# Kernel tuning notes

Hardware: AMD Instinct MI355X
Metric: run time of the kernel (lower is better)

Reference implementation:

```python
import jax, jax.numpy as jnp
import numpy as np
from jax import lax

G, K, C_IN, C_FEAT, H, W, B = 8, 6, 512, 256, 64, 64, 1


def apply_offset(offset):
    # offset: [N, 2, H, W] pixel-space offsets -> sampling grid [N, H, W, 2] in [-1, 1]
    # channel 0 displaces x (width), channel 1 displaces y (height), matching the
    # reversed-meshgrid logic of the original torch apply_offset.
    n, _, h, w = offset.shape
    jj = jnp.arange(w, dtype=offset.dtype)[None, None, :]
    ii = jnp.arange(h, dtype=offset.dtype)[None, :, None]
    gx = (jj + offset[:, 0]) / ((w - 1.0) / 2.0) - 1.0
    gy = (ii + offset[:, 1]) / ((h - 1.0) / 2.0) - 1.0
    return jnp.stack([gx, gy], axis=-1)


def grid_sample_border(img, grid):
    # img: [N, C, H, W], grid: [N, H, W, 2] in [-1, 1]
    # Bilinear, padding_mode='border', align_corners=False (torch grid_sample default).
    n, c, h, w = img.shape
    x = jnp.clip((grid[..., 0] + 1.0) * w * 0.5 - 0.5, 0.0, w - 1.0)
    y = jnp.clip((grid[..., 1] + 1.0) * h * 0.5 - 0.5, 0.0, h - 1.0)
    x0 = jnp.floor(x)
    y0 = jnp.floor(y)
    wx = (x - x0)[:, None]  # [N,1,H,W]
    wy = (y - y0)[:, None]
    x0i = x0.astype(jnp.int32)
    y0i = y0.astype(jnp.int32)
    x1i = jnp.minimum(x0i + 1, w - 1)
    y1i = jnp.minimum(y0i + 1, h - 1)

    def gather(im, yi, xi):  # im [C,H,W]; yi, xi [H,W]
        return im[:, yi, xi]

    g = jax.vmap(gather)
    v00 = g(img, y0i, x0i)
    v01 = g(img, y0i, x1i)
    v10 = g(img, y1i, x0i)
    v11 = g(img, y1i, x1i)
    return (1.0 - wy) * ((1.0 - wx) * v00 + wx * v01) + wy * ((1.0 - wx) * v10 + wx * v11)


def setup_inputs() -> dict:
    key = jax.random.key(0)
    ks = jax.random.split(key, 11)
    s = 0.02
    return {
        "gar_feat": jax.random.normal(ks[0], (B, C_FEAT, H, W), jnp.float32),
        "cond_feat": jax.random.normal(ks[1], (B, C_FEAT, H, W), jnp.float32),
        "mask": jax.random.uniform(ks[2], (B, G, C_FEAT), dtype=jnp.float32),
        "W1": jax.random.normal(ks[3], (G, 128, C_IN, 3, 3), jnp.float32) * s,
        "b1": jax.random.normal(ks[4], (G, 128), jnp.float32) * s,
        "W2": jax.random.normal(ks[5], (G, 64, 128, 3, 3), jnp.float32) * s,
        "b2": jax.random.normal(ks[6], (G, 64), jnp.float32) * s,
        "W3": jax.random.normal(ks[7], (G, 32, 64, 3, 3), jnp.float32) * s,
        "b3": jax.random.normal(ks[8], (G, 32), jnp.float32) * s,
        "W4": jax.random.normal(ks[9], (G, 3 * K, 32, 3, 3), jnp.float32) * s,
        "b4": jax.random.normal(ks[10], (G, 3 * K), jnp.float32) * s,
    }


def reference(gar_feat, cond_feat, mask, W1, b1, W2, b2, W3, b3, W4, b4):
    b, c, h, w = gar_feat.shape
    g = W1.shape[0]
    k = W4.shape[1] // 3
    inp = jnp.concatenate([gar_feat, cond_feat], axis=1)  # [B, 2C, H, W]

    def conv(x, wgt, bias):
        return lax.conv_general_dilated(
            x, wgt, (1, 1), 'SAME', dimension_numbers=('NCHW', 'OIHW', 'NCHW')
        ) + bias[None, :, None, None]

    def lrelu(x):
        return jnp.where(x >= 0, x, 0.1 * x)

    def group_net(w1, bb1, w2, bb2, w3, bb3, w4, bb4):
        hid = lrelu(conv(inp, w1, bb1))
        hid = lrelu(conv(hid, w2, bb2))
        hid = lrelu(conv(hid, w3, bb3))
        return conv(hid, w4, bb4)  # [B, 3k, H, W]

    oa = jax.vmap(group_net)(W1, b1, W2, b2, W3, b3, W4, b4)  # [G, B, 3k, H, W]
    attn = jax.nn.softmax(oa[:, :, 2 * k:], axis=0)           # softmax across groups: [G,B,k,H,W]
    off = oa[:, :, :2 * k].reshape(g, b * k, 2, h, w)
    grid = jax.vmap(apply_offset)(off)                        # [G, B*k, H, W, 2]

    rep = jnp.repeat(gar_feat, k, axis=0)                     # [B*k, C, H, W]

    def warp_group(grid_g, attn_g, mask_g):
        samp = grid_sample_border(rep, grid_g).reshape(b, k, c, h, w)
        wfeat = jnp.sum(samp * attn_g[:, :, None], axis=1)    # [B, C, H, W]
        return wfeat * mask_g[:, :, None, None]

    warped = jax.vmap(warp_group)(grid, attn, jnp.transpose(mask, (1, 0, 2)))
    return jnp.sum(warped, axis=0)  # [B, C, H, W]
```

## Files before the change

kernel.cpp:

```cpp
#include <hip/hip_runtime.h>
#include <hip/hip_bf16.h>

typedef __hip_bfloat16 bf16;
typedef unsigned short ushort8v __attribute__((ext_vector_type(8)));
typedef short  s16x4  __attribute__((ext_vector_type(4)));
typedef short  bf16x8 __attribute__((ext_vector_type(8)));
typedef float  f32x4  __attribute__((ext_vector_type(4)));

#define HW 4096
#define IMG_W 64

__device__ __forceinline__ float bfbits2f(unsigned short u) {
    return __uint_as_float(((unsigned int)u) << 16);
}
__device__ __forceinline__ short f2bs(float f) {
    bf16 h = __float2bfloat16(f);
    return *reinterpret_cast<short*>(&h);
}

__device__ __forceinline__ void gl_lds16(const void* g, void* s) {
    __builtin_amdgcn_global_load_lds(
        (const __attribute__((address_space(1))) unsigned int*)g,
        (__attribute__((address_space(3))) unsigned int*)s, 16, 0, 0);
}

__device__ void pack_input_dev(const float* __restrict__ gar,
                               const float* __restrict__ cond,
                               short* __restrict__ outp, int bx2, float* tile)
{
    int bx = bx2 & 127;
    int by = bx2 >> 7;
    int tx = threadIdx.x & 31;
    int ty = threadIdx.x >> 5;
#pragma unroll
    for (int i = 0; i < 4; ++i) {
        int c = by * 32 + ty + i * 8;
        const float* src = (c < 256) ? (gar + (size_t)c * HW)
                                     : (cond + (size_t)(c - 256) * HW);
        tile[(ty + i * 8) * 33 + tx] = src[bx * 32 + tx];
    }
    __syncthreads();
#pragma unroll
    for (int i = 0; i < 4; ++i) {
        int p = bx * 32 + ty + i * 8;
        outp[((size_t)by * 4096 + p) * 32 + tx] = f2bs(tile[tx * 33 + ty + i * 8]);
    }
}

template<int CIN, int CREAL, int BN, int NT, bool COAL>
__device__ void pack_w_dev(const float* __restrict__ wgt, char* __restrict__ wp,
                           int bx, short* sT)
{
    constexpr int NCC  = CIN / 32;
    constexpr int BLKB = 9 * 4 * BN * 16;

    const int t  = threadIdx.x;
    const int cc = bx % NCC;
    const int nt = (bx / NCC) % NT;
    const int g  = bx / (NT * NCC);

    for (int i = t; i < BLKB / 8; i += 256)
        reinterpret_cast<s16x4*>(sT)[i] = s16x4{0, 0, 0, 0};
    __syncthreads();

    int ocmax = CREAL - nt * BN; if (ocmax > BN) ocmax = BN;
    const size_t base = ((size_t)(g * CREAL + nt * BN) * CIN + cc * 32) * 9;
    for (int i = t; i < ocmax * 288; i += 256) {
        int oc = i / 288;
        int r  = i % 288;
        int ic = r / 9, tap = r % 9;
        size_t idx;
        if (COAL) idx = (size_t)(((tap * BN + oc) * 4 + (ic >> 3)) * 8 + (ic & 7));
        else      idx = (size_t)(((tap * 4 + (ic >> 3)) * BN + oc) * 8 + (ic & 7));
        sT[idx] = f2bs(wgt[base + (size_t)oc * CIN * 9 + r]);
    }
    __syncthreads();

    const s16x4* src = reinterpret_cast<const s16x4*>(sT);
    s16x4* dst = reinterpret_cast<s16x4*>(wp + (size_t)bx * BLKB);
    for (int i = t; i < BLKB / 8; i += 256)
        dst[i] = src[i];
}

__global__ __launch_bounds__(256)
void pack_all(const float* __restrict__ gar, const float* __restrict__ cond,
              const float* __restrict__ W1, const float* __restrict__ W2,
              const float* __restrict__ W3, const float* __restrict__ W4,
              short* inp_t, char* W1p, char* W2p, char* W3p, char* W4p)
{
    __shared__ __align__(16) short sbuf[9 * 4 * 64 * 8];
    int bx = blockIdx.x;
    if (bx < 256)      pack_w_dev<512, 128, 64, 2, true >(W1, W1p, bx,       sbuf);
    else if (bx < 288) pack_w_dev<128,  64, 64, 1, false>(W2, W2p, bx - 256, sbuf);
    else if (bx < 304) pack_w_dev< 64,  32, 32, 1, false>(W3, W3p, bx - 288, sbuf);
    else if (bx < 312) pack_w_dev< 32,  18, 32, 1, false>(W4, W4p, bx - 304, sbuf);
    else pack_input_dev(gar, cond, inp_t, bx - 312, (float*)sbuf);
}

template<int ICP, int CREAL, int BN, int ROWS, int OF, int NT, int NW, int PIPE,
         bool PIXMAJ_OUT, bool LEAKY, bool OUT_F32>
__global__ __launch_bounds__(NW * 64, 2)
void conv_mfma(const short* __restrict__ inp, const char* __restrict__ wp,
               const float* __restrict__ bias, void* __restrict__ outv)
{
    constexpr int NCC  = ICP / 32;
    constexpr int HALO = ROWS + 2;
    constexpr int NPT  = 4096 / (ROWS * 64);
    constexpr int BLKB = 9 * 4 * BN * 16;
    constexpr int RNDS = BLKB / 1024;
    constexpr int NBUF = (PIPE && NCC > 1) ? 2 : 1;
    constexpr int SMAX = (HALO + NW - 1) / NW;

    __shared__ __align__(16) short sA[HALO][4][68][8];
    __shared__ __align__(16) char  sBraw[NBUF][BLKB];

    const int b  = blockIdx.x;
    const int g  = b & 7;
    const int r_ = b >> 3;
    const int pt = r_ % NPT;
    const int nt = r_ / NPT;
    const int r0 = pt * ROWS;

    const int t    = threadIdx.x;
    const int wave = t >> 6, lane = t & 63;
    const int l15  = lane & 15, quad = lane >> 4;

    int row_l, ocw;
    if (NW == 8) {
        if (ROWS == 4) { row_l = wave >> 1; ocw = (wave & 1) * (BN / 2); }
        else           { row_l = wave >> 2; ocw = (wave & 3) * (BN / 4); }
    } else {
        row_l = (ROWS == 4) ? wave : (wave & 1);
        ocw   = (ROWS == 4) ? 0 : (wave >> 1) * (BN / 2);
    }

    const size_t gpix = (ICP == 512) ? 0 : ((size_t)g * 4096);
    const char*  wb   = wp + (size_t)((g * NT + nt) * NCC) * BLKB;

    const int acol = t & 63;
    const int r2   = t >> 6;

    bf16x8 pre[SMAX][4];

    auto stageA_load = [&](int cc) {
#pragma unroll
        for (int s = 0; s < SMAX; ++s) {
            int j = r2 + s * NW;
            if (j < HALO) {
                int gy = r0 - 1 + j;
                if (gy >= 0 && gy < 64) {
                    const short* sp = inp + ((gpix + gy * 64 + acol) * ICP + cc * 32);
#pragma unroll
                    for (int q = 0; q < 4; ++q)
                        pre[s][q] = *reinterpret_cast<const bf16x8*>(sp + q * 8);
                } else {
#pragma unroll
                    for (int q = 0; q < 4; ++q)
                        pre[s][q] = bf16x8{0, 0, 0, 0, 0, 0, 0, 0};
                }
            }
        }
    };
    auto stageA_write = [&]() {
#pragma unroll
        for (int s = 0; s < SMAX; ++s) {
            int j = r2 + s * NW;
            if (j < HALO) {
#pragma unroll
                for (int q = 0; q < 4; ++q)
                    *reinterpret_cast<bf16x8*>(&sA[j][q][acol + 1][0]) = pre[s][q];
            }
        }
    };
    auto stageB = [&](int cc) {
        const char* wsrc = wb + (size_t)cc * BLKB;
        char* sbb = (char*)sBraw[(NBUF == 2) ? (cc & 1) : 0];
        for (int r = wave; r < RNDS; r += NW)
            gl_lds16(wsrc + r * 1024 + lane * 16, sbb + r * 1024);
    };

    f32x4 acc[OF][4];
#pragma unroll
    for (int o = 0; o < OF; ++o)
#pragma unroll
        for (int p = 0; p < 4; ++p)
#pragma unroll
            for (int r = 0; r < 4; ++r) acc[o][p][r] = 0.f;

    if (t < HALO * 8) {
        int row = t >> 3, q = (t >> 1) & 3, cp = (t & 1) ? 65 : 0;
        *reinterpret_cast<bf16x8*>(&sA[row][q][cp][0]) =
            bf16x8{0, 0, 0, 0, 0, 0, 0, 0};
    }

    stageB(0);
    stageA_load(0);
    stageA_write();

    for (int cc = 0; cc < NCC; ++cc) {
        __syncthreads();
        if (cc + 1 < NCC) {
            if (PIPE) stageB(cc + 1);
            stageA_load(cc + 1);
        }
        const bf16x8* sBv = reinterpret_cast<const bf16x8*>(
            sBraw[(NBUF == 2) ? (cc & 1) : 0]);

#pragma unroll
        for (int dy = 0; dy < 3; ++dy) {
#pragma unroll
            for (int dx = 0; dx < 3; ++dx) {
                bf16x8 pF[4];
#pragma unroll
                for (int p = 0; p < 4; ++p)
                    pF[p] = *reinterpret_cast<const bf16x8*>(
                        &sA[row_l + dy][quad][p * 16 + l15 + dx][0]);
                bf16x8 wF[OF];
#pragma unroll
                for (int o = 0; o < OF; ++o)
                    wF[o] = sBv[((dy * 3 + dx) * 4 + quad) * BN + ocw + o * 16 + l15];
#pragma unroll
                for (int o = 0; o < OF; ++o)
#pragma unroll
                    for (int p = 0; p < 4; ++p)
                        acc[o][p] = __builtin_amdgcn_mfma_f32_16x16x32_bf16(
                            wF[o], pF[p], acc[o][p], 0, 0, 0);
            }
        }
        __syncthreads();
        if (cc + 1 < NCC) {
            if (!PIPE) stageB(cc + 1);
            stageA_write();
        }
    }

    const int prow = r0 + row_l;
#pragma unroll
    for (int o = 0; o < OF; ++o)
#pragma unroll
        for (int reg = 0; reg < 4; ++reg) {
            const int ocl = ocw + o * 16 + quad * 4 + reg;
            const int ocg = nt * BN + ocl;
            if (ocg < CREAL) {
                const float bv = bias[g * CREAL + ocg];
                if (PIXMAJ_OUT) {
                    short* outp = (short*)outv;
                    const size_t pixbase = ((size_t)g * 4096 + prow * 64);
#pragma unroll
                    for (int p = 0; p < 4; ++p) {
                        float v = acc[o][p][reg] + bv;
                        if (LEAKY) v = v >= 0.f ? v : 0.1f * v;
                        outp[(pixbase + p * 16 + l15) * (NT * BN) + ocg] = f2bs(v);
                    }
                } else if (OUT_F32) {
                    float* outp = (float*)outv;
                    const size_t base = ((size_t)(g * CREAL + ocg)) * HW + prow * IMG_W;
#pragma unroll
                    for (int p = 0; p < 4; ++p) {
                        float v = acc[o][p][reg] + bv;
                        if (LEAKY) v = v >= 0.f ? v : 0.1f * v;
                        outp[base + p * 16 + l15] = v;
                    }
                } else {
                    short* outp = (short*)outv;
                    const size_t base = ((size_t)(g * CREAL + ocg)) * HW + prow * IMG_W;
#pragma unroll
                    for (int p = 0; p < 4; ++p) {
                        float v = acc[o][p][reg] + bv;
                        if (LEAKY) v = v >= 0.f ? v : 0.1f * v;
                        outp[base + p * 16 + l15] = f2bs(v);
                    }
                }
            }
        }
}

__global__ __launch_bounds__(256, 2)
void conv1_direct(const short* __restrict__ inp, const char* __restrict__ wp,
                  const float* __restrict__ bias, short* __restrict__ outp)
{
    __shared__ __align__(16) short sA[2][4][66][4][8];

    const int b  = blockIdx.x;
    const int g  = b & 7;
    const int r_ = b >> 3;
    const int pt = r_ & 31;
    const int nt = r_ >> 5;
    const int r0 = pt * 2;

    const int t    = threadIdx.x;
    const int wave = t >> 6, lane = t & 63;
    const int l15  = lane & 15, quad = lane >> 4;

    const int row_l = wave & 1;
    const int ocw   = (wave >> 1) * 32;

    const short* wb    = (const short*)wp + (size_t)(g * 2 + nt) * 16 * 18432;
    const short* wlane = wb + ((size_t)(ocw + l15) * 4 + quad) * 8;

    auto stageDMA = [&](int cc, int buf) {
        int gy = r0 - 1 + wave;
        if (gy >= 0 && gy < 64) {
            const short* src = inp + ((size_t)cc * 4096 + (size_t)gy * 64) * 32
                                   + (size_t)lane * 8;
#pragma unroll
            for (int c4 = 0; c4 < 4; ++c4)
                gl_lds16(src + c4 * 512, &sA[buf][wave][1 + c4 * 16][0][0]);
        }
    };

    bf16x8 wA[9][2], wB[9][2];
    auto loadW_into = [&](int cc, bf16x8 (&w)[9][2]) {
        const short* ws = wlane + (size_t)cc * 18432;
#pragma unroll
        for (int tap = 0; tap < 9; ++tap)
#pragma unroll
            for (int o = 0; o < 2; ++o)
                w[tap][o] = *reinterpret_cast<const bf16x8*>(
                    ws + tap * 2048 + o * 512);
    };

    f32x4 acc[2][4];
#pragma unroll
    for (int o = 0; o < 2; ++o)
#pragma unroll
        for (int p = 0; p < 4; ++p)
#pragma unroll
            for (int r = 0; r < 4; ++r) acc[o][p][r] = 0.f;

    loadW_into(0, wA);
    stageDMA(0, 0);
    if (t < 64) {
        int buf = t >> 5, row = (t >> 3) & 3, q = (t >> 1) & 3;
        int col = (t & 1) ? 65 : 0;
        *reinterpret_cast<bf16x8*>(&sA[buf][row][col][q][0]) =
            bf16x8{0, 0, 0, 0, 0, 0, 0, 0};
    }
    if (r0 == 0 || r0 == 62) {
        int zr = (r0 == 0) ? 0 : 3;
        for (int i = t; i < 2 * 66 * 4; i += 256) {
            int buf = i / 264, rem = i % 264;
            *reinterpret_cast<bf16x8*>(&sA[buf][zr][rem >> 2][rem & 3][0]) =
                bf16x8{0, 0, 0, 0, 0, 0, 0, 0};
        }
    }

    auto body = [&](int cc, int cur, bf16x8 (&wuse)[9][2], bf16x8 (&wld)[9][2]) {
        __syncthreads();
        if (cc + 1 < 16) {
            stageDMA(cc + 1, cur ^ 1);
            loadW_into(cc + 1, wld);
        }
#pragma unroll
        for (int dy = 0; dy < 3; ++dy)
#pragma unroll
            for (int dx = 0; dx < 3; ++dx) {
                bf16x8 pF[4];
#pragma unroll
                for (int p = 0; p < 4; ++p)
                    pF[p] = *reinterpret_cast<const bf16x8*>(
                        &sA[cur][row_l + dy][p * 16 + l15 + dx][quad][0]);
#pragma unroll
                for (int o = 0; o < 2; ++o)
#pragma unroll
                    for (int p = 0; p < 4; ++p)
                        acc[o][p] = __builtin_amdgcn_mfma_f32_16x16x32_bf16(
                            wuse[dy * 3 + dx][o], pF[p], acc[o][p], 0, 0, 0);
            }
    };

    for (int c2 = 0; c2 < 16; c2 += 2) {
        body(c2,     0, wA, wB);
        body(c2 + 1, 1, wB, wA);
    }

    const int prow = r0 + row_l;
    const size_t pixbase = (size_t)g * 4096 + (size_t)prow * 64;
#pragma unroll
    for (int o = 0; o < 2; ++o)
#pragma unroll
        for (int reg = 0; reg < 4; ++reg) {
            const int ocg = nt * 64 + ocw + o * 16 + quad * 4 + reg;
            const float bv = bias[g * 128 + ocg];
#pragma unroll
            for (int p = 0; p < 4; ++p) {
                float v = acc[o][p][reg] + bv;
                v = v >= 0.f ? v : 0.1f * v;
                outp[(pixbase + p * 16 + l15) * 128 + ocg] = f2bs(v);
            }
        }
}

__global__ __launch_bounds__(256, 2)
void conv1_of4(const short* __restrict__ inp, const char* __restrict__ wp,
               float* __restrict__ part0, float* __restrict__ part1)
{
    __shared__ __align__(16) short sA[2][4][66][4][8];

    const int b  = blockIdx.x;
    const int g  = b & 7;
    const int r_ = b >> 3;
    const int pt = r_ & 31;
    const int ks = (r_ >> 5) & 1;
    const int r0 = pt * 2;
    const int cc0 = ks * 8;

    const int t    = threadIdx.x;
    const int wave = t >> 6, lane = t & 63;
    const int l15  = lane & 15, quad = lane >> 4;

    const int row_l = wave & 1;
    const int ntw   = wave >> 1;

    const short* wb    = (const short*)wp + (size_t)(g * 2 + ntw) * 16 * 18432;
    const short* wlane = wb + ((size_t)l15 * 4 + quad) * 8;

    auto stageDMA = [&](int cc, int buf) {
        int gy = r0 - 1 + wave;
        if (gy >= 0 && gy < 64) {
            const short* src = inp + ((size_t)cc * 4096 + (size_t)gy * 64) * 32
                                   + (size_t)lane * 8;
#pragma unroll
            for (int c4 = 0; c4 < 4; ++c4)
                gl_lds16(src + c4 * 512, &sA[buf][wave][1 + c4 * 16][0][0]);
        }
    };

    f32x4 acc[4][4];
#pragma unroll
    for (int o = 0; o < 4; ++o)
#pragma unroll
        for (int p = 0; p < 4; ++p)
#pragma unroll
            for (int r = 0; r < 4; ++r) acc[o][p][r] = 0.f;

    stageDMA(cc0, 0);
    if (t < 64) {
        int buf = t >> 5, row = (t >> 3) & 3, q = (t >> 1) & 3;
        int col = (t & 1) ? 65 : 0;
        *reinterpret_cast<bf16x8*>(&sA[buf][row][col][q][0]) =
            bf16x8{0, 0, 0, 0, 0, 0, 0, 0};
    }
    if (r0 == 0 || r0 == 62) {
        int zr = (r0 == 0) ? 0 : 3;
        for (int i = t; i < 2 * 66 * 4; i += 256) {
            int buf = i / 264, rem = i % 264;
            *reinterpret_cast<bf16x8*>(&sA[buf][zr][rem >> 2][rem & 3][0]) =
                bf16x8{0, 0, 0, 0, 0, 0, 0, 0};
        }
    }

    auto body = [&](int i, int cur) {
        const int cc = cc0 + i;
        __syncthreads();
        if (i + 1 < 8) stageDMA(cc + 1, cur ^ 1);
        const short* wcc = wlane + (size_t)cc * 18432;

        bf16x8 w[9][4];
#pragma unroll
        for (int tap = 0; tap < 9; ++tap)
#pragma unroll
            for (int o = 0; o < 4; ++o)
                w[tap][o] = *reinterpret_cast<const bf16x8*>(
                    wcc + tap * 2048 + o * 512);

#pragma unroll
        for (int dy = 0; dy < 3; ++dy)
#pragma unroll
            for (int dx = 0; dx < 3; ++dx) {
                bf16x8 pF[4];
#pragma unroll
                for (int p = 0; p < 4; ++p)
                    pF[p] = *reinterpret_cast<const bf16x8*>(
                        &sA[cur][row_l + dy][p * 16 + l15 + dx][quad][0]);
#pragma unroll
                for (int o = 0; o < 4; ++o)
#pragma unroll
                    for (int p = 0; p < 4; ++p)
                        acc[o][p] = __builtin_amdgcn_mfma_f32_16x16x32_bf16(
                            w[dy * 3 + dx][o], pF[p], acc[o][p], 0, 0, 0);
            }
    };

    for (int i2 = 0; i2 < 8; i2 += 2) {
        body(i2,     0);
        body(i2 + 1, 1);
    }

    float* pp = ks ? part1 : part0;
    const int prow = r0 + row_l;
    const size_t pixbase = (size_t)g * 4096 + (size_t)prow * 64;
#pragma unroll
    for (int o = 0; o < 4; ++o)
#pragma unroll
        for (int reg = 0; reg < 4; ++reg) {
            const int ocg = ntw * 64 + o * 16 + quad * 4 + reg;
#pragma unroll
            for (int p = 0; p < 4; ++p)
                pp[(pixbase + p * 16 + l15) * 128 + ocg] = acc[o][p][reg];
        }
}

__global__ __launch_bounds__(256)
void finalize_conv1(const float* __restrict__ p0, const float* __restrict__ p1,
                    const float* __restrict__ bias, short* __restrict__ outp)
{
    const size_t i8 = ((size_t)blockIdx.x * 256 + threadIdx.x) * 8;
    const int oc0 = (int)(i8 & 127);
    const int g   = (int)(i8 >> 19);
    float4 a0 = *reinterpret_cast<const float4*>(p0 + i8);
    float4 a1 = *reinterpret_cast<const float4*>(p0 + i8 + 4);
    float4 b0 = *reinterpret_cast<const float4*>(p1 + i8);
    float4 b1 = *reinterpret_cast<const float4*>(p1 + i8 + 4);
    float4 c0 = *reinterpret_cast<const float4*>(bias + g * 128 + oc0);
    float4 c1 = *reinterpret_cast<const float4*>(bias + g * 128 + oc0 + 4);
    float v[8] = {a0.x + b0.x + c0.x, a0.y + b0.y + c0.y,
                  a0.z + b0.z + c0.z, a0.w + b0.w + c0.w,
                  a1.x + b1.x + c1.x, a1.y + b1.y + c1.y,
                  a1.z + b1.z + c1.z, a1.w + b1.w + c1.w};
    ushort8v r;
#pragma unroll
    for (int j = 0; j < 8; ++j) {
        float x = v[j] >= 0.f ? v[j] : 0.1f * v[j];
        r[j] = (unsigned short)f2bs(x);
    }
    *reinterpret_cast<ushort8v*>(outp + i8) = r;
}

__global__ __launch_bounds__(256)
void warp_combine_kernel(const float* __restrict__ oa,
                         const short* __restrict__ inp_t,
                         const float* __restrict__ mask,
                         float* __restrict__ out)
{
    __shared__ __align__(16) float4 sWts[8][6][8];
    __shared__ __align__(16) int4   sIdx[8][6][8];

    const int t = threadIdx.x;

    if (t < 48) {
        int lp = t / 6;
        int k  = t % 6;
        int p  = blockIdx.x * 8 + lp;
        int x  = p & 63, y = p >> 6;

        float l[8];
        float m = -1e30f;
#pragma unroll
        for (int g = 0; g < 8; ++g) {
            l[g] = oa[(size_t)(g * 18 + 12 + k) * HW + p];
            m = fmaxf(m, l[g]);
        }
        float s = 0.f;
#pragma unroll
        for (int g = 0; g < 8; ++g) { l[g] = __expf(l[g] - m); s += l[g]; }
        float inv = 1.f / s;

#pragma unroll
        for (int g = 0; g < 8; ++g) {
            float a  = l[g] * inv;
            float ox = oa[(size_t)(g * 18 + 2 * k)     * HW + p];
            float oy = oa[(size_t)(g * 18 + 2 * k + 1) * HW + p];
            float sx = fminf(fmaxf(((float)x + ox) * (64.f / 63.f) - 0.5f, 0.f), 63.f);
            float sy = fminf(fmaxf(((float)y + oy) * (64.f / 63.f) - 0.5f, 0.f), 63.f);
            float fx0 = floorf(sx), fy0 = floorf(sy);
            int   x0 = (int)fx0,    y0i = (int)fy0;
            float wx = sx - fx0,    wy = sy - fy0;
            int   x1 = min(x0 + 1, 63), y1 = min(y0i + 1, 63);
            sWts[lp][k][g] = make_float4(a * (1.f - wy) * (1.f - wx),
                                         a * (1.f - wy) * wx,
                                         a * wy * (1.f - wx),
                                         a * wy * wx);
            sIdx[lp][k][g] = make_int4(y0i * 64 + x0, y0i * 64 + x1,
                                       y1  * 64 + x0, y1  * 64 + x1);
        }
    }
    __syncthreads();

    const int lp = t >> 5;
    const int p  = blockIdx.x * 8 + lp;
    const int c0 = (t & 31) * 8;
    const short* ipc = inp_t + (size_t)(c0 >> 5) * (4096 * 32) + (c0 & 31);

    float acc[8];
#pragma unroll
    for (int j = 0; j < 8; ++j) acc[j] = 0.f;

    for (int g = 0; g < 8; ++g) {
        float4 m0 = *reinterpret_cast<const float4*>(mask + g * 256 + c0);
        float4 m1 = *reinterpret_cast<const float4*>(mask + g * 256 + c0 + 4);
        float mk[8] = {m0.x, m0.y, m0.z, m0.w, m1.x, m1.y, m1.z, m1.w};
#pragma unroll
        for (int k = 0; k < 6; ++k) {
            float4 w  = sWts[lp][k][g];
            int4   id = sIdx[lp][k][g];
            ushort8v v00 = *reinterpret_cast<const ushort8v*>(ipc + (size_t)id.x * 32);
            ushort8v v01 = *reinterpret_cast<const ushort8v*>(ipc + (size_t)id.y * 32);
            ushort8v v10 = *reinterpret_cast<const ushort8v*>(ipc + (size_t)id.z * 32);
            ushort8v v11 = *reinterpret_cast<const ushort8v*>(ipc + (size_t)id.w * 32);
#pragma unroll
            for (int j = 0; j < 8; ++j) {
                float sv = w.x * bfbits2f(v00[j]) + w.y * bfbits2f(v01[j])
                         + w.z * bfbits2f(v10[j]) + w.w * bfbits2f(v11[j]);
                acc[j] = fmaf(mk[j], sv, acc[j]);
            }
        }
    }
#pragma unroll
    for (int j = 0; j < 8; ++j)
        out[(size_t)(c0 + j) * HW + p] = acc[j];
}

extern "C" void kernel_launch(void* const* d_in, const int* in_sizes, int n_in,
                              void* d_out, int out_size, void* d_ws, size_t ws_size,
                              hipStream_t stream)
{
    (void)in_sizes; (void)n_in; (void)out_size;
    const float* gar  = (const float*)d_in[0];
    const float* cond = (const float*)d_in[1];
    const float* mask = (const float*)d_in[2];
    const float* W1   = (const float*)d_in[3];
    const float* b1   = (const float*)d_in[4];
    const float* W2   = (const float*)d_in[5];
    const float* b2   = (const float*)d_in[6];
    const float* W3   = (const float*)d_in[7];
    const float* b3   = (const float*)d_in[8];
    const float* W4   = (const float*)d_in[9];
    const float* b4   = (const float*)d_in[10];
    float* out = (float*)d_out;

    char* ws = (char*)d_ws;
    short* inp_t  = (short*)(ws);
    char*  W1p    = ws + (4u << 20);
    short* hid2_t = (short*)(ws + (4u << 20));
    short* hid3_t = (short*)(ws + (8u << 20));
    float* oa     = (float*)(ws + (10u << 20) + (512u << 10));
    char*  W2p    = ws + (14u << 20);
    char*  W3p    = ws + (15u << 20) + (512u << 10);
    char*  W4p    = ws + (16u << 20);
    short* hid1_t = (short*)(ws + (17u << 20));
    float* part0  = (float*)(ws + (28u << 20));
    float* part1  = (float*)(ws + (44u << 20));

    pack_all<<<2360, 256, 0, stream>>>(gar, cond, W1, W2, W3, W4,
                                       inp_t, W1p, W2p, W3p, W4p);

    if (ws_size >= ((size_t)60 << 20)) {
        conv1_of4<<<512, 256, 0, stream>>>(inp_t, W1p, part0, part1);
        finalize_conv1<<<2048, 256, 0, stream>>>(part0, part1, b1, hid1_t);
    } else {
        conv1_direct<<<512, 256, 0, stream>>>(inp_t, W1p, b1, hid1_t);
    }
    conv_mfma<128, 64, 64, 2, 1, 1, 8, 1, true, true, false>
        <<<256, 512, 0, stream>>>(hid1_t, W2p, b2, hid2_t);
    conv_mfma<64, 32, 32, 2, 1, 1, 4, 1, true, true, false>
        <<<256, 256, 0, stream>>>(hid2_t, W3p, b3, hid3_t);
    conv_mfma<32, 18, 32, 2, 1, 1, 4, 1, false, false, true>
        <<<256, 256, 0, stream>>>(hid3_t, W4p, b4, oa);

    warp_combine_kernel<<<512, 256, 0, stream>>>(oa, inp_t, mask, out);
}
```

Baseline: 210.1 us.

## Use 4-row, 512-thread conv1 blocks with double-buffered weight prefetch

The first 3x3 convolution kernel now covers four output rows per block with eight waves instead of two rows with four waves. This lets a staged input halo of six rows serve four output rows, cutting redundant LDS staging and global input reads. Weights are no longer loaded as all nine taps up front; a two-slot register ring prefetches the next tap's weights while the current tap's MFMAs run, split by a sched_barrier. The aim is lower register pressure and better latency hiding, but each block is now larger and the grid smaller (256 blocks), and the wrap-around prefetch at tap 8 reads into the next channel chunk's weights.

```diff
diff --git a/kernel.cpp b/kernel.cpp
--- a/kernel.cpp
+++ b/kernel.cpp
@@ -391,38 +391,40 @@
         }
 }
 
-__global__ __launch_bounds__(256, 2)
-void conv1_of4(const short* __restrict__ inp, const char* __restrict__ wp,
-               float* __restrict__ part0, float* __restrict__ part1)
-{
-    __shared__ __align__(16) short sA[2][4][66][4][8];
+__global__ __launch_bounds__(512, 2)
+void conv1_r4(const short* __restrict__ inp, const char* __restrict__ wp,
+              float* __restrict__ part0, float* __restrict__ part1)
+{
+    __shared__ __align__(16) short sA[2][6][66][4][8];
 
     const int b  = blockIdx.x;
     const int g  = b & 7;
     const int r_ = b >> 3;
-    const int pt = r_ & 31;
-    const int ks = (r_ >> 5) & 1;
-    const int r0 = pt * 2;
+    const int pt = r_ & 15;
+    const int ks = (r_ >> 4) & 1;
+    const int r0 = pt * 4;
     const int cc0 = ks * 8;
 
     const int t    = threadIdx.x;
     const int wave = t >> 6, lane = t & 63;
     const int l15  = lane & 15, quad = lane >> 4;
 
-    const int row_l = wave & 1;
-    const int ntw   = wave >> 1;
+    const int row_l = wave & 3;
+    const int ntw   = wave >> 2;
 
     const short* wb    = (const short*)wp + (size_t)(g * 2 + ntw) * 16 * 18432;
     const short* wlane = wb + ((size_t)l15 * 4 + quad) * 8;
 
     auto stageDMA = [&](int cc, int buf) {
-        int gy = r0 - 1 + wave;
-        if (gy >= 0 && gy < 64) {
-            const short* src = inp + ((size_t)cc * 4096 + (size_t)gy * 64) * 32
-                                   + (size_t)lane * 8;
-#pragma unroll
-            for (int c4 = 0; c4 < 4; ++c4)
-                gl_lds16(src + c4 * 512, &sA[buf][wave][1 + c4 * 16][0][0]);
+        if (wave < 6) {
+            int gy = r0 - 1 + wave;
+            if (gy >= 0 && gy < 64) {
+                const short* src = inp + ((size_t)cc * 4096 + (size_t)gy * 64) * 32
+                                       + (size_t)lane * 8;
+#pragma unroll
+                for (int c4 = 0; c4 < 4; ++c4)
+                    gl_lds16(src + c4 * 512, &sA[buf][wave][1 + c4 * 16][0][0]);
+            }
         }
     };
 
@@ -435,56 +437,59 @@
             for (int r = 0; r < 4; ++r) acc[o][p][r] = 0.f;
 
     stageDMA(cc0, 0);
-    if (t < 64) {
-        int buf = t >> 5, row = (t >> 3) & 3, q = (t >> 1) & 3;
+    if (t < 96) {
+        int buf = t / 48, rem = t % 48;
+        int row = rem >> 3, q = (rem >> 1) & 3;
         int col = (t & 1) ? 65 : 0;
         *reinterpret_cast<bf16x8*>(&sA[buf][row][col][q][0]) =
             bf16x8{0, 0, 0, 0, 0, 0, 0, 0};
     }
-    if (r0 == 0 || r0 == 62) {
-        int zr = (r0 == 0) ? 0 : 3;
-        for (int i = t; i < 2 * 66 * 4; i += 256) {
+    if (r0 == 0 || r0 == 60) {
+        int zr = (r0 == 0) ? 0 : 5;
+        for (int i = t; i < 2 * 66 * 4; i += 512) {
             int buf = i / 264, rem = i % 264;
             *reinterpret_cast<bf16x8*>(&sA[buf][zr][rem >> 2][rem & 3][0]) =
                 bf16x8{0, 0, 0, 0, 0, 0, 0, 0};
         }
     }
 
-    auto body = [&](int i, int cur) {
+    bf16x8 w[2][4];
+#pragma unroll
+    for (int o = 0; o < 4; ++o)
+        w[0][o] = *reinterpret_cast<const bf16x8*>(
+            wlane + (size_t)cc0 * 18432 + o * 512);
+
+    auto body = [&](int i, int cur, int par) {
         const int cc = cc0 + i;
+        const short* wcc = wlane + (size_t)cc * 18432;
         __syncthreads();
         if (i + 1 < 8) stageDMA(cc + 1, cur ^ 1);
-        const short* wcc = wlane + (size_t)cc * 18432;
-
-        bf16x8 w[9][4];
-#pragma unroll
-        for (int tap = 0; tap < 9; ++tap)
+#pragma unroll
+        for (int tap = 0; tap < 9; ++tap) {
+            const int cb = (tap + par) & 1, nb = cb ^ 1;
+            const int dy = tap / 3, dx = tap % 3;
+            const short* nsrc = wcc + (size_t)(tap + 1) * 2048;
 #pragma unroll
             for (int o = 0; o < 4; ++o)
-                w[tap][o] = *reinterpret_cast<const bf16x8*>(
-                    wcc + tap * 2048 + o * 512);
-
-#pragma unroll
-        for (int dy = 0; dy < 3; ++dy)
-#pragma unroll
-            for (int dx = 0; dx < 3; ++dx) {
-                bf16x8 pF[4];
+                w[nb][o] = *reinterpret_cast<const bf16x8*>(nsrc + o * 512);
+            __builtin_amdgcn_sched_barrier(0);
+            bf16x8 pF[4];
+#pragma unroll
+            for (int p = 0; p < 4; ++p)
+                pF[p] = *reinterpret_cast<const bf16x8*>(
+                    &sA[cur][row_l + dy][p * 16 + l15 + dx][quad][0]);
+#pragma unroll
+            for (int o = 0; o < 4; ++o)
 #pragma unroll
                 for (int p = 0; p < 4; ++p)
-                    pF[p] = *reinterpret_cast<const bf16x8*>(
-                        &sA[cur][row_l + dy][p * 16 + l15 + dx][quad][0]);
-#pragma unroll
-                for (int o = 0; o < 4; ++o)
-#pragma unroll
-                    for (int p = 0; p < 4; ++p)
-                        acc[o][p] = __builtin_amdgcn_mfma_f32_16x16x32_bf16(
-                            w[dy * 3 + dx][o], pF[p], acc[o][p], 0, 0, 0);
-            }
+                    acc[o][p] = __builtin_amdgcn_mfma_f32_16x16x32_bf16(
+                        w[cb][o], pF[p], acc[o][p], 0, 0, 0);
+        }
     };
 
     for (int i2 = 0; i2 < 8; i2 += 2) {
-        body(i2,     0);
-        body(i2 + 1, 1);
+        body(i2,     0, 0);
+        body(i2 + 1, 1, 1);
     }
 
     float* pp = ks ? part1 : part0;
@@ -646,7 +651,7 @@
                                        inp_t, W1p, W2p, W3p, W4p);
 
     if (ws_size >= ((size_t)60 << 20)) {
-        conv1_of4<<<512, 256, 0, stream>>>(inp_t, W1p, part0, part1);
+        conv1_r4<<<256, 512, 0, stream>>>(inp_t, W1p, part0, part1);
         finalize_conv1<<<2048, 256, 0, stream>>>(part0, part1, b1, hid1_t);
     } else {
         conv1_direct<<<512, 256, 0, stream>>>(inp_t, W1p, b1, hid1_t);
```

Result: faster. 203.8 us (-3.0%).
